# Optimization experiments

Hardware: AMD Instinct MI355X
Metric: run time of the kernel (lower is better)

## Reference

```python
import jax, jax.numpy as jnp
import numpy as np
import math

B, S, D, H, L, DFF = 64, 512, 512, 8, 2, 1024
DK = D // H
NEG = -1e32
LN_EPS = 1e-5


def cosine_pos_emb(seqlen, d_model):
    # pe[:,0::2]=sin(pos*div), pe[:,1::2]=cos(pos*div) -- fully overwrites the randn init
    pos = jnp.arange(seqlen, dtype=jnp.float32)[:, None]
    div = jnp.exp(jnp.arange(0, d_model, 2, dtype=jnp.float32) * (-math.log(10000.0) / d_model))
    ang = pos * div  # [S, D/2]
    return jnp.stack([jnp.sin(ang), jnp.cos(ang)], axis=-1).reshape(seqlen, d_model)


def layernorm(x, g, b):
    m = jnp.mean(x, axis=-1, keepdims=True)
    v = jnp.var(x, axis=-1, keepdims=True)
    return g * (x - m) * jax.lax.rsqrt(v + LN_EPS) + b


def setup_inputs() -> dict:
    key = jax.random.key(0)
    ks = jax.random.split(key, 8)
    sc = 0.02
    inp = {
        'q_embed_data': jax.random.normal(ks[0], (B, S, D), jnp.float32),
        'qa_embed_data': jax.random.normal(ks[1], (B, S, D), jnp.float32),
        'forget_rate': jax.random.uniform(ks[2], (B, 1, S, 1), jnp.float32),
        # per-block params, leading dim = n_blocks (kq_same=1: q uses k_linear)
        'Wk': jax.random.normal(ks[3], (L, D, D), jnp.float32) * sc,
        'bk': jnp.zeros((L, D), jnp.float32),
        'Wv': jax.random.normal(ks[4], (L, D, D), jnp.float32) * sc,
        'bv': jnp.zeros((L, D), jnp.float32),
        'Wo': jax.random.normal(ks[5], (L, D, D), jnp.float32) * sc,
        'bo': jnp.zeros((L, D), jnp.float32),
        'ln1_g': jnp.ones((L, D), jnp.float32),
        'ln1_b': jnp.zeros((L, D), jnp.float32),
        'W1': jax.random.normal(ks[6], (L, D, DFF), jnp.float32) * sc,
        'b1': jnp.zeros((L, DFF), jnp.float32),
        'W2': jax.random.normal(ks[7], (L, DFF, D), jnp.float32) * sc,
        'b2': jnp.zeros((L, D), jnp.float32),
        'ln2_g': jnp.ones((L, D), jnp.float32),
        'ln2_b': jnp.zeros((L, D), jnp.float32),
    }
    return inp


def reference(q_embed_data, qa_embed_data, forget_rate, Wk, bk, Wv, bv, Wo, bo,
              ln1_g, ln1_b, W1, b1, W2, b2, ln2_g, ln2_b):
    pe = cosine_pos_emb(S, D)
    x = q_embed_data + pe  # query/key stream
    y = qa_embed_data + pe  # value stream (fixed across blocks)
    # mask=0 path: np.triu(ones, k=0) == 0 -> strictly lower-triangular allowed
    allow = jnp.tril(jnp.ones((S, S), dtype=bool), -1)
    scale = 1.0 / math.sqrt(DK)
    for i in range(L):
        qk = (x @ Wk[i] + bk[i]).reshape(B, S, H, DK).transpose(0, 2, 1, 3)  # [B,H,S,dk]
        v = (y @ Wv[i] + bv[i]).reshape(B, S, H, DK).transpose(0, 2, 1, 3)
        scores = jnp.einsum('bhqd,bhkd->bhqk', qk, qk) * scale
        scores = scores * forget_rate  # [B,1,S,1] broadcasts over heads and keys
        scores = jnp.where(allow, scores, NEG)
        p = jax.nn.softmax(scores, axis=-1)
        p = p.at[:, :, 0, :].set(0.0)  # zero_pad: first query row zeroed
        attn = jnp.einsum('bhqk,bhkd->bhqd', p, v).transpose(0, 2, 1, 3).reshape(B, S, D)
        attn = attn @ Wo[i] + bo[i]
        x = layernorm(x + attn, ln1_g[i], ln1_b[i])
        ff = jax.nn.relu(x @ W1[i] + b1[i]) @ W2[i] + b2[i]
        x = layernorm(x + ff, ln2_g[i], ln2_b[i])
    return x
```

## Files before the change

### kernel.cpp

```cpp
#include <hip/hip_runtime.h>
#include <cstdio>

#define B_   64
#define S_   512
#define D_   512
#define H_   8
#define DK_  64
#define DFF_ 1024
#define L_   2
#define BS_  (B_ * S_)

typedef __attribute__((ext_vector_type(8))) short bf16x8;
typedef __attribute__((ext_vector_type(4))) short bf16x4;
typedef __attribute__((ext_vector_type(4))) float f32x4;

__device__ inline short f2bf(float f) {
  unsigned u = __float_as_uint(f);
  u = u + 0x7FFF + ((u >> 16) & 1);
  return (short)(u >> 16);
}
__device__ inline float bf2f(short s) {
  return __uint_as_float(((unsigned)(unsigned short)s) << 16);
}

__device__ inline void gl_lds16(const short* g, void* lds_base) {
  __builtin_amdgcn_global_load_lds(
      (const __attribute__((address_space(1))) void*)g,
      (__attribute__((address_space(3))) void*)lds_base, 16, 0, 0);
}

__global__ void pe_kernel(float* __restrict__ pe) {
  int idx = blockIdx.x * 256 + threadIdx.x;
  int s = idx >> 9, d = idx & 511;
  float dv = __expf((float)(d & ~1) * (-9.210340371976184f / (float)D_));
  float ang = (float)s * dv;
  pe[idx] = (d & 1) ? cosf(ang) : sinf(ang);
}

__global__ __launch_bounds__(256) void prep_kernel(
    const float* __restrict__ q, const float* __restrict__ qa,
    const float* __restrict__ pe,
    short* __restrict__ xb, short* __restrict__ yb) {
  size_t base = ((size_t)blockIdx.x * 256 + threadIdx.x) * 8;
  int sd = (int)(base & (size_t)(S_ * D_ - 1));
  f32x4 p0 = *(const f32x4*)(pe + sd);
  f32x4 p1 = *(const f32x4*)(pe + sd + 4);
  f32x4 q0 = *(const f32x4*)(q + base);
  f32x4 q1 = *(const f32x4*)(q + base + 4);
  f32x4 a0 = *(const f32x4*)(qa + base);
  f32x4 a1 = *(const f32x4*)(qa + base + 4);
  bf16x8 xv, yv;
#pragma unroll
  for (int i = 0; i < 4; ++i) {
    xv[i] = f2bf(q0[i] + p0[i]);
    yv[i] = f2bf(a0[i] + p0[i]);
  }
#pragma unroll
  for (int i = 0; i < 4; ++i) {
    xv[4 + i] = f2bf(q1[i] + p1[i]);
    yv[4 + i] = f2bf(a1[i] + p1[i]);
  }
  *(bf16x8*)(xb + base) = xv;
  *(bf16x8*)(yb + base) = yv;
}

struct TrArgs {
  const float* src[10];
  short* dst[10];
  int R[10], C[10];
};
__global__ __launch_bounds__(256) void tr_w_all(TrArgs a) {
  const int slot = blockIdx.z;
  const int R = a.R[slot], C = a.C[slot];
  const int c0 = blockIdx.x * 64, r0 = blockIdx.y * 64;
  if (c0 >= C || r0 >= R) return;
  const float* __restrict__ src = a.src[slot];
  short* __restrict__ dst = a.dst[slot];
  __shared__ short Ts[64][72];
  const int t = threadIdx.x;
#pragma unroll
  for (int it = 0; it < 2; ++it) {
    int c2 = it * 256 + t;
    int srow = c2 >> 3, schunk = c2 & 7;
    const float* sp = src + (size_t)(r0 + srow) * C + c0 + schunk * 8;
    f32x4 a0 = *(const f32x4*)sp;
    f32x4 a1 = *(const f32x4*)(sp + 4);
#pragma unroll
    for (int k = 0; k < 4; ++k) Ts[srow][schunk * 8 + k] = f2bf(a0[k]);
#pragma unroll
    for (int k = 0; k < 4; ++k) Ts[srow][schunk * 8 + 4 + k] = f2bf(a1[k]);
  }
  __syncthreads();
#pragma unroll
  for (int it = 0; it < 2; ++it) {
    int c2 = it * 256 + t;
    int orow = c2 >> 3, ochunk = c2 & 7;
    bf16x8 vv;
#pragma unroll
    for (int k = 0; k < 8; ++k) vv[k] = Ts[ochunk * 8 + k][orow];
    *(bf16x8*)(dst + (size_t)(c0 + orow) * R + r0 + ochunk * 8) = vv;
  }
}

__global__ __launch_bounds__(512, 2) void gemm_bt(
    const short* __restrict__ A, const short* __restrict__ BT,
    const float* __restrict__ bias, short* __restrict__ Cb,
    int M, int N, int K, int relu, int bias_row, int nx, int xmaj)
{
  const int nwg = gridDim.x;
  const int cpx = nwg >> 3;
  const int l = (blockIdx.x & 7) * cpx + (blockIdx.x >> 3);
  int bcol, brow;
  if (xmaj) { bcol = l % nx; brow = l / nx; }
  else      { int ny = nwg / nx; brow = l % ny; bcol = l / ny; }

  __shared__ __align__(16) short As[2][256 * 64];
  __shared__ __align__(16) short Bs[2][256 * 64];
  const int t = threadIdx.x;
  const int w = t >> 6, lane = t & 63, lr = lane & 15, lk = lane >> 4;
  const int wm = w >> 2, wn = w & 3;

  const f32x4 vzero = {0.f, 0.f, 0.f, 0.f};
  f32x4 acc[8][4];
#pragma unroll
  for (int m = 0; m < 8; ++m)
#pragma unroll
    for (int n = 0; n < 4; ++n) acc[m][n] = vzero;

  const short* Abase = A + (size_t)brow * 256 * K;
  const short* Bbase = BT + (size_t)bcol * 256 * K;

  auto stageH = [&](short* lds, const short* gsrc, int half, int k0) {
#pragma unroll
    for (int it = 0; it < 2; ++it) {
      int c = it * 512 + t;
      int cb = it * 512 + w * 64;
      int row = half * 128 + (c >> 3);
      int seg = (c & 7) ^ (row & 7);
      gl_lds16(gsrc + (size_t)row * K + k0 + seg * 8,
               (char*)lds + (size_t)(half * 1024 + cb) * 16);
    }
  };
  auto ldfrag = [&](const short* lds, int row, int s) -> bf16x8 {
    int chunk = row * 8 + (s ^ (row & 7));
    return *(const bf16x8*)((const char*)lds + (size_t)chunk * 16);
  };

  const int T = K >> 6;
  stageH(&As[0][0], Abase, 0, 0);
  stageH(&As[0][0], Abase, 1, 0);
  stageH(&Bs[0][0], Bbase, 0, 0);
  stageH(&Bs[0][0], Bbase, 1, 0);

  for (int ti = 0; ti < T; ++ti) {
    const int cbuf = ti & 1, obuf = cbuf ^ 1;
    asm volatile("s_waitcnt vmcnt(0)" ::: "memory");
    asm volatile("s_barrier" ::: "memory");

    if (ti + 1 < T) {
      int k1 = (ti + 1) * 64;
      stageH(&As[obuf][0], Abase, 0, k1);
      stageH(&As[obuf][0], Abase, 1, k1);
      stageH(&Bs[obuf][0], Bbase, 0, k1);
      stageH(&Bs[obuf][0], Bbase, 1, k1);
    }

    bf16x8 bf[4][2];
#pragma unroll
    for (int n = 0; n < 4; ++n)
#pragma unroll
      for (int kk = 0; kk < 2; ++kk)
        bf[n][kk] = ldfrag(&Bs[cbuf][0], wn * 64 + n * 16 + lr, kk * 4 + lk);

#pragma unroll
    for (int p = 0; p < 4; ++p) {
      bf16x8 af[2][2];
#pragma unroll
      for (int mm = 0; mm < 2; ++mm)
#pragma unroll
        for (int kk = 0; kk < 2; ++kk)
          af[mm][kk] = ldfrag(&As[cbuf][0], wm * 128 + (p * 2 + mm) * 16 + lr, kk * 4 + lk);
      __builtin_amdgcn_sched_barrier(0);
      __builtin_amdgcn_s_setprio(1);
#pragma unroll
      for (int mm = 0; mm < 2; ++mm)
#pragma unroll
        for (int n = 0; n < 4; ++n)
#pragma unroll
          for (int kk = 0; kk < 2; ++kk)
            acc[p * 2 + mm][n] = __builtin_amdgcn_mfma_f32_16x16x32_bf16(
                bf[n][kk], af[mm][kk], acc[p * 2 + mm][n], 0, 0, 0);
      __builtin_amdgcn_s_setprio(0);
      __builtin_amdgcn_sched_barrier(0);
      asm volatile("s_barrier" ::: "memory");
    }
  }

#pragma unroll
  for (int m = 0; m < 8; ++m) {
    int row = brow * 256 + wm * 128 + m * 16 + lr;
    float brv = (bias && bias_row) ? bias[row] : 0.f;
    size_t rb = (size_t)row * N;
#pragma unroll
    for (int n = 0; n < 4; ++n) {
      int colb = bcol * 256 + wn * 64 + n * 16 + lk * 4;
      f32x4 bv4;
      if (bias && !bias_row) bv4 = *(const f32x4*)(bias + colb);
      else { bv4[0] = brv; bv4[1] = brv; bv4[2] = brv; bv4[3] = brv; }
      bf16x4 ov;
#pragma unroll
      for (int j = 0; j < 4; ++j) {
        float vv = acc[m][n][j] + bv4[j];
        if (relu) vv = fmaxf(vv, 0.f);
        ov[j] = f2bf(vv);
      }
      *(bf16x4*)(Cb + rb + colb) = ov;
    }
  }
}

template<int P>
__device__ __forceinline__ void attn_body(
    const short* __restrict__ qk, const short* __restrict__ vT,
    const float* __restrict__ fr, short* __restrict__ out,
    short (*Pl)[552], float (*redsum)[32][4],
    int h, int b, int w, int lr, int lk)
{
  constexpr int qo0 = 32 * P, qo1 = 32 * (15 - P);
  constexpr int c0 = 2 * P + 2;
  constexpr int colb1 = c0 * 16;
  constexpr int n0 = P + 1;
  constexpr int n1 = 16 - P;

  const size_t qk_head = (size_t)b * S_ * D_ + (size_t)h * DK_;
  const float scale = 0.125f;

  bf16x8 qf0[2][2], qf1[2][2];
#pragma unroll
  for (int qt = 0; qt < 2; ++qt)
#pragma unroll
    for (int ks = 0; ks < 2; ++ks) {
      qf0[qt][ks] = *(const bf16x8*)(qk + qk_head + (size_t)(qo0 + qt * 16 + lr) * D_ + ks * 32 + lk * 8);
      qf1[qt][ks] = *(const bf16x8*)(qk + qk_head + (size_t)(qo1 + qt * 16 + lr) * D_ + ks * 32 + lk * 8);
    }

  float frv0[2], frv1[2];
#pragma unroll
  for (int qt = 0; qt < 2; ++qt) {
    frv0[qt] = scale * fr[(size_t)b * S_ + qo0 + qt * 16 + lr];
    frv1[qt] = scale * fr[(size_t)b * S_ + qo1 + qt * 16 + lr];
  }

  const f32x4 vzero = {0.f, 0.f, 0.f, 0.f};
  f32x4 acc[9][2];
#pragma unroll
  for (int i = 0; i < 9; ++i) { acc[i][0] = vzero; acc[i][1] = vzero; }

  const int nfr = (w < 2) ? 9 : 8;
  const short* kqbase = qk + qk_head + (size_t)lr * D_ + lk * 8;
  auto kfoff = [&](int i) -> size_t {
    int f = w + 4 * i;
    int kt = (f < c0) ? f : f - c0;
    return (size_t)kt * 16 * D_;
  };
  bf16x8 kreg[4][2];
#pragma unroll
  for (int i = 0; i < 4; ++i) {
    if (i < nfr) {
      const short* p = kqbase + kfoff(i);
      kreg[i][0] = *(const bf16x8*)p;
      kreg[i][1] = *(const bf16x8*)(p + 32);
    }
  }
  __builtin_amdgcn_sched_barrier(0);
#pragma unroll
  for (int i = 0; i < 9; ++i) {
    if (i < nfr) {
      const int f = w + 4 * i;
      __builtin_amdgcn_s_setprio(1);
      if (f < c0) {
#pragma unroll
        for (int ks = 0; ks < 2; ++ks) {
          acc[i][0] = __builtin_amdgcn_mfma_f32_16x16x32_bf16(kreg[i & 3][ks], qf0[0][ks], acc[i][0], 0, 0, 0);
          acc[i][1] = __builtin_amdgcn_mfma_f32_16x16x32_bf16(kreg[i & 3][ks], qf0[1][ks], acc[i][1], 0, 0, 0);
        }
      } else {
#pragma unroll
        for (int ks = 0; ks < 2; ++ks) {
          acc[i][0] = __builtin_amdgcn_mfma_f32_16x16x32_bf16(kreg[i & 3][ks], qf1[0][ks], acc[i][0], 0, 0, 0);
          acc[i][1] = __builtin_amdgcn_mfma_f32_16x16x32_bf16(kreg[i & 3][ks], qf1[1][ks], acc[i][1], 0, 0, 0);
        }
      }
      __builtin_amdgcn_s_setprio(0);
      __builtin_amdgcn_sched_barrier(0);
      if (i + 4 < nfr) {
        const short* p = kqbase + kfoff(i + 4);
        kreg[i & 3][0] = *(const bf16x8*)p;
        kreg[i & 3][1] = *(const bf16x8*)(p + 32);
      }
      __builtin_amdgcn_sched_barrier(0);
    }
  }

  const int uqt0 = w & 1, udh0 = w >> 1;
  const int uqt1 = w >> 1, udh1 = w & 1;
  const short* vu0 = vT + (size_t)(h * DK_ + udh0 * 32 + lr) * BS_ + (size_t)b * S_ + lk * 8;
  const short* vu1 = vT + (size_t)(h * DK_ + udh1 * 32 + lr) * BS_ + (size_t)b * S_ + lk * 8;
  bf16x8 vfB[3][2][2];
#pragma unroll
  for (int kb = 0; kb < 3; ++kb) {
    if (kb < n0) {
#pragma unroll
      for (int n = 0; n < 2; ++n)
        vfB[kb][0][n] = *(const bf16x8*)(vu0 + (size_t)n * 16 * BS_ + kb * 32);
    }
    if (kb < n1) {
#pragma unroll
      for (int n = 0; n < 2; ++n)
        vfB[kb][1][n] = *(const bf16x8*)(vu1 + (size_t)n * 16 * BS_ + kb * 32);
    }
  }
  __builtin_amdgcn_sched_barrier(0);

  float rs00 = 0.f, rs01 = 0.f, rs10 = 0.f, rs11 = 0.f;
#pragma unroll
  for (int frag = 0; frag < 34; ++frag) {
    if ((frag & 3) == w) {
      const int i = frag >> 2;
      const int tl = (frag < c0) ? 0 : 1;
      const int kt = tl ? frag - c0 : frag;
      const int kbase = kt * 16 + lk * 4;
      const int colb = (tl ? colb1 : 0) + kbase;
#pragma unroll
      for (int qt = 0; qt < 2; ++qt) {
        int qrow = (tl ? qo1 : qo0) + qt * 16 + lr;
        float fv = tl ? frv1[qt] : frv0[qt];
        bf16x4 pk;
        float rs = 0.f;
#pragma unroll
        for (int j = 0; j < 4; ++j) {
          float e = (kbase + j < qrow) ? __expf(acc[i][qt][j] * fv) : 0.f;
          rs += e;
          pk[j] = f2bf(e);
        }
        *(bf16x4*)&Pl[qt * 16 + lr][colb] = pk;
        if (tl == 0) { if (qt == 0) rs00 += rs; else rs01 += rs; }
        else         { if (qt == 0) rs10 += rs; else rs11 += rs; }
      }
    }
  }

#pragma unroll
  for (int msk = 16; msk < 64; msk <<= 1) {
    rs00 += __shfl_xor(rs00, msk);
    rs01 += __shfl_xor(rs01, msk);
    rs10 += __shfl_xor(rs10, msk);
    rs11 += __shfl_xor(rs11, msk);
  }
  if (lk == 0) {
    redsum[0][lr][w] = rs00;
    redsum[0][16 + lr][w] = rs01;
    redsum[1][lr][w] = rs10;
    redsum[1][16 + lr][w] = rs11;
  }
  __syncthreads();

  const short* prow0 = &Pl[uqt0 * 16 + lr][lk * 8];
  const short* prow1 = &Pl[uqt1 * 16 + lr][colb1 + lk * 8];
  f32x4 oacc0[2] = {vzero, vzero}, oacc1[2] = {vzero, vzero};
  bf16x8 paB[2][2];
  paB[0][0] = *(const bf16x8*)prow0;
  paB[0][1] = *(const bf16x8*)prow1;

#pragma unroll
  for (int kb = 0; kb < 16; ++kb) {
    const int sc = kb % 3, pc = kb & 1, pn = pc ^ 1;
    if (kb + 1 < n0) paB[pn][0] = *(const bf16x8*)(prow0 + (kb + 1) * 32);
    if (kb + 1 < n1) paB[pn][1] = *(const bf16x8*)(prow1 + (kb + 1) * 32);
    __builtin_amdgcn_sched_barrier(0);
    __builtin_amdgcn_s_setprio(1);
    if (kb < n0) {
#pragma unroll
      for (int n = 0; n < 2; ++n)
        oacc0[n] = __builtin_amdgcn_mfma_f32_16x16x32_bf16(paB[pc][0], vfB[sc][0][n], oacc0[n], 0, 0, 0);
    }
    if (kb < n1) {
#pragma unroll
      for (int n = 0; n < 2; ++n)
        oacc1[n] = __builtin_amdgcn_mfma_f32_16x16x32_bf16(paB[pc][1], vfB[sc][1][n], oacc1[n], 0, 0, 0);
    }
    __builtin_amdgcn_s_setprio(0);
    __builtin_amdgcn_sched_barrier(0);
    if (kb + 3 < n0) {
#pragma unroll
      for (int n = 0; n < 2; ++n)
        vfB[sc][0][n] = *(const bf16x8*)(vu0 + (size_t)n * 16 * BS_ + (kb + 3) * 32);
    }
    if (kb + 3 < n1) {
#pragma unroll
      for (int n = 0; n < 2; ++n)
        vfB[sc][1][n] = *(const bf16x8*)(vu1 + (size_t)n * 16 * BS_ + (kb + 3) * 32);
    }
    __builtin_amdgcn_sched_barrier(0);
  }

  {
    float invd[4];
#pragma unroll
    for (int j = 0; j < 4; ++j) {
      int row = uqt0 * 16 + lk * 4 + j;
      float ds = redsum[0][row][0] + redsum[0][row][1] + redsum[0][row][2] + redsum[0][row][3];
      invd[j] = ds > 0.f ? 1.f / ds : 0.f;
    }
#pragma unroll
    for (int n = 0; n < 2; ++n)
#pragma unroll
      for (int j = 0; j < 4; ++j) {
        int qrow = qo0 + uqt0 * 16 + lk * 4 + j;
        out[qk_head + (size_t)qrow * D_ + udh0 * 32 + n * 16 + lr] = f2bf(oacc0[n][j] * invd[j]);
      }
  }
  {
    float invd[4];
#pragma unroll
    for (int j = 0; j < 4; ++j) {
      int row = uqt1 * 16 + lk * 4 + j;
      float ds = redsum[1][row][0] + redsum[1][row][1] + redsum[1][row][2] + redsum[1][row][3];
      invd[j] = ds > 0.f ? 1.f / ds : 0.f;
    }
#pragma unroll
    for (int n = 0; n < 2; ++n)
#pragma unroll
      for (int j = 0; j < 4; ++j) {
        int qrow = qo1 + uqt1 * 16 + lk * 4 + j;
        out[qk_head + (size_t)qrow * D_ + udh1 * 32 + n * 16 + lr] = f2bf(oacc1[n][j] * invd[j]);
      }
  }
}

__global__ __launch_bounds__(256, 3) void attn_kernel(
    const short* __restrict__ qk, const short* __restrict__ vT,
    const float* __restrict__ fr, short* __restrict__ out)
{
  const int hw = blockIdx.x;
  const int l = (hw & 7) * 512 + (hw >> 3);
  const int p = l & 7, hb = l >> 3;
  const int h = hb & 7, b = hb >> 3;
  const int t = threadIdx.x;
  const int w = t >> 6, lr = t & 15, lk = (t & 63) >> 4;

  __shared__ __align__(16) short Pl[32][552];
  __shared__ __align__(16) float redsum[2][32][4];

  switch (p) {
    case 0: attn_body<0>(qk, vT, fr, out, Pl, redsum, h, b, w, lr, lk); break;
    case 1: attn_body<1>(qk, vT, fr, out, Pl, redsum, h, b, w, lr, lk); break;
    case 2: attn_body<2>(qk, vT, fr, out, Pl, redsum, h, b, w, lr, lk); break;
    case 3: attn_body<3>(qk, vT, fr, out, Pl, redsum, h, b, w, lr, lk); break;
    case 4: attn_body<4>(qk, vT, fr, out, Pl, redsum, h, b, w, lr, lk); break;
    case 5: attn_body<5>(qk, vT, fr, out, Pl, redsum, h, b, w, lr, lk); break;
    case 6: attn_body<6>(qk, vT, fr, out, Pl, redsum, h, b, w, lr, lk); break;
    case 7: attn_body<7>(qk, vT, fr, out, Pl, redsum, h, b, w, lr, lk); break;
  }
}

template<int FINAL>
__global__ __launch_bounds__(256) void ln_res_t(
    const short* __restrict__ xin, const short* __restrict__ add,
    const float* __restrict__ g, const float* __restrict__ bb,
    short* __restrict__ xbout, float* __restrict__ fout)
{
  const int row = blockIdx.x * 4 + (threadIdx.x >> 6);
  const int lane = threadIdx.x & 63;
  const size_t base = (size_t)row * D_ + lane * 8;

  bf16x8 xv = *(const bf16x8*)(xin + base);
  bf16x8 av = *(const bf16x8*)(add + base);
  float vals[8];
#pragma unroll
  for (int i = 0; i < 8; ++i) vals[i] = bf2f(xv[i]) + bf2f(av[i]);

  float s = 0.f, sq = 0.f;
#pragma unroll
  for (int i = 0; i < 8; ++i) { s += vals[i]; sq += vals[i] * vals[i]; }
#pragma unroll
  for (int m = 1; m < 64; m <<= 1) { s += __shfl_xor(s, m); sq += __shfl_xor(sq, m); }

  float mean = s * (1.f / D_);
  float var = sq * (1.f / D_) - mean * mean;
  float rstd = rsqrtf(var + 1e-5f);

  int col = lane * 8;
  if (FINAL) {
    f32x4 o0, o1;
#pragma unroll
    for (int i = 0; i < 8; ++i) {
      float vv = g[col + i] * (vals[i] - mean) * rstd + bb[col + i];
      if (i < 4) o0[i] = vv; else o1[i - 4] = vv;
    }
    *(f32x4*)(fout + base) = o0;
    *(f32x4*)(fout + base + 4) = o1;
  } else {
    bf16x8 ob;
#pragma unroll
    for (int i = 0; i < 8; ++i)
      ob[i] = f2bf(g[col + i] * (vals[i] - mean) * rstd + bb[col + i]);
    *(bf16x8*)(xbout + base) = ob;
  }
}

extern "C" void kernel_launch(void* const* d_in, const int* in_sizes, int n_in,
                              void* d_out, int out_size, void* d_ws, size_t ws_size,
                              hipStream_t stream) {
  const float* q_emb = (const float*)d_in[0];
  const float* qa_emb = (const float*)d_in[1];
  const float* frate = (const float*)d_in[2];
  const float* Wk = (const float*)d_in[3];
  const float* bk = (const float*)d_in[4];
  const float* Wv = (const float*)d_in[5];
  const float* bv = (const float*)d_in[6];
  const float* Wo = (const float*)d_in[7];
  const float* bo = (const float*)d_in[8];
  const float* ln1g = (const float*)d_in[9];
  const float* ln1b = (const float*)d_in[10];
  const float* W1 = (const float*)d_in[11];
  const float* b1 = (const float*)d_in[12];
  const float* W2 = (const float*)d_in[13];
  const float* b2 = (const float*)d_in[14];
  const float* ln2g = (const float*)d_in[15];
  const float* ln2b = (const float*)d_in[16];
  float* x = (float*)d_out;

  char* ws = (char*)d_ws;
  size_t off = 0;
  auto alloc = [&](size_t bytes) -> void* {
    void* p = ws + off;
    off += (bytes + 255) & ~(size_t)255;
    return p;
  };
  const size_t MTOK = (size_t)BS_;
  float* pe    = (float*)alloc((size_t)S_ * D_ * 4);
  short* xb    = (short*)alloc(MTOK * D_ * 2);
  short* yb    = (short*)alloc(MTOK * D_ * 2);
  short* qkb   = (short*)alloc(MTOK * D_ * 2);
  short* vTb   = (short*)alloc(MTOK * D_ * 2);
  short* ff1b  = (short*)alloc(MTOK * DFF_ * 2);
  short* attnb = ff1b;
  short* goutb = qkb;
  short* wT[L_][5];
  for (int i = 0; i < L_; ++i) {
    wT[i][0] = (short*)alloc((size_t)D_ * D_ * 2);
    wT[i][1] = (short*)alloc((size_t)D_ * D_ * 2);
    wT[i][2] = (short*)alloc((size_t)D_ * D_ * 2);
    wT[i][3] = (short*)alloc((size_t)D_ * DFF_ * 2);
    wT[i][4] = (short*)alloc((size_t)DFF_ * D_ * 2);
  }
  if (off > ws_size) {
    fprintf(stderr, "parKT: workspace overflow: need %zu have %zu\n", off, ws_size);
    return;
  }

  pe_kernel<<<(S_ * D_) / 256, 256, 0, stream>>>(pe);
  prep_kernel<<<(int)(MTOK * D_ / (256 * 8)), 256, 0, stream>>>(q_emb, qa_emb, pe, xb, yb);

  TrArgs ta;
  for (int i = 0; i < L_; ++i) {
    ta.src[i * 5 + 0] = Wk + (size_t)i * D_ * D_;  ta.dst[i * 5 + 0] = wT[i][0]; ta.R[i * 5 + 0] = D_;   ta.C[i * 5 + 0] = D_;
    ta.src[i * 5 + 1] = Wv + (size_t)i * D_ * D_;  ta.dst[i * 5 + 1] = wT[i][1]; ta.R[i * 5 + 1] = D_;   ta.C[i * 5 + 1] = D_;
    ta.src[i * 5 + 2] = Wo + (size_t)i * D_ * D_;  ta.dst[i * 5 + 2] = wT[i][2]; ta.R[i * 5 + 2] = D_;   ta.C[i * 5 + 2] = D_;
    ta.src[i * 5 + 3] = W1 + (size_t)i * D_ * DFF_; ta.dst[i * 5 + 3] = wT[i][3]; ta.R[i * 5 + 3] = D_;   ta.C[i * 5 + 3] = DFF_;
    ta.src[i * 5 + 4] = W2 + (size_t)i * DFF_ * D_; ta.dst[i * 5 + 4] = wT[i][4]; ta.R[i * 5 + 4] = DFF_; ta.C[i * 5 + 4] = D_;
  }
  tr_w_all<<<dim3(DFF_ / 64, DFF_ / 64, 10), 256, 0, stream>>>(ta);

  const int M = (int)MTOK;
  for (int i = 0; i < L_; ++i) {
    gemm_bt<<<(M / 256) * (D_ / 256), 512, 0, stream>>>(xb, wT[i][0], bk + (size_t)i * D_, qkb, M, D_, D_, 0, 0, D_ / 256, 1);
    gemm_bt<<<(D_ / 256) * (M / 256), 512, 0, stream>>>(wT[i][1], yb, bv + (size_t)i * D_, vTb, D_, M, D_, 0, 1, M / 256, 0);
    attn_kernel<<<(S_ / 64) * H_ * B_, 256, 0, stream>>>(qkb, vTb, frate, attnb);
    gemm_bt<<<(M / 256) * (D_ / 256), 512, 0, stream>>>(attnb, wT[i][2], bo + (size_t)i * D_, goutb, M, D_, D_, 0, 0, D_ / 256, 1);
    ln_res_t<0><<<M / 4, 256, 0, stream>>>(xb, goutb, ln1g + (size_t)i * D_, ln1b + (size_t)i * D_, xb, nullptr);
    gemm_bt<<<(M / 256) * (DFF_ / 256), 512, 0, stream>>>(xb, wT[i][3], b1 + (size_t)i * DFF_, ff1b, M, DFF_, D_, 1, 0, DFF_ / 256, 1);
    gemm_bt<<<(M / 256) * (D_ / 256), 512, 0, stream>>>(ff1b, wT[i][4], b2 + (size_t)i * D_, goutb, M, D_, DFF_, 0, 0, D_ / 256, 1);
    if (i == L_ - 1)
      ln_res_t<1><<<M / 4, 256, 0, stream>>>(xb, goutb, ln2g + (size_t)i * D_, ln2b + (size_t)i * D_, nullptr, x);
    else
      ln_res_t<0><<<M / 4, 256, 0, stream>>>(xb, goutb, ln2g + (size_t)i * D_, ln2b + (size_t)i * D_, xb, nullptr);
  }
}
```

Measured before the change: 735.0 us.

## Merge QK and V projections into one GEMM launch and pipeline K-halves

The QK and transposed-V projection GEMMs now run as a single grouped launch: each workgroup picks its problem from a pair of argument structs by block index. The GEMM main loop is restructured so LDS is laid out per 32-wide K half with a new swizzle. The next tile's loads are issued in quarter-steps interleaved with the MFMA blocks, with partial vmcnt waits instead of a full drain. This aims to overlap global-to-LDS traffic with compute and to cut one launch plus its tail per layer. The cost is more complex waitcnt accounting, which risks reading data before it has arrived if the counts are wrong.

```diff
diff --git a/kernel.cpp b/kernel.cpp
--- a/kernel.cpp
+++ b/kernel.cpp
@@ -102,20 +102,33 @@
   }
 }
 
-__global__ __launch_bounds__(512, 2) void gemm_bt(
-    const short* __restrict__ A, const short* __restrict__ BT,
-    const float* __restrict__ bias, short* __restrict__ Cb,
-    int M, int N, int K, int relu, int bias_row, int nx, int xmaj)
+struct GArgs {
+  const short* A; const short* BT; const float* bias; short* Cb;
+  int M, N, K, relu, bias_row, nx, xmaj, nblk;
+};
+__global__ __launch_bounds__(512, 2) void gemm_bt2(GArgs g0, GArgs g1)
 {
   const int nwg = gridDim.x;
   const int cpx = nwg >> 3;
   const int l = (blockIdx.x & 7) * cpx + (blockIdx.x >> 3);
+
+  const short* A; const short* BT; const float* bias; short* Cb;
+  int N, K, relu, bias_row, nx, xmaj, ll, nb;
+  if (l < g0.nblk) {
+    A = g0.A; BT = g0.BT; bias = g0.bias; Cb = g0.Cb;
+    N = g0.N; K = g0.K; relu = g0.relu; bias_row = g0.bias_row;
+    nx = g0.nx; xmaj = g0.xmaj; ll = l; nb = g0.nblk;
+  } else {
+    A = g1.A; BT = g1.BT; bias = g1.bias; Cb = g1.Cb;
+    N = g1.N; K = g1.K; relu = g1.relu; bias_row = g1.bias_row;
+    nx = g1.nx; xmaj = g1.xmaj; ll = l - g0.nblk; nb = g1.nblk;
+  }
   int bcol, brow;
-  if (xmaj) { bcol = l % nx; brow = l / nx; }
-  else      { int ny = nwg / nx; brow = l % ny; bcol = l / ny; }
-
-  __shared__ __align__(16) short As[2][256 * 64];
-  __shared__ __align__(16) short Bs[2][256 * 64];
+  if (xmaj) { bcol = ll % nx; brow = ll / nx; }
+  else      { int ny = nb / nx; brow = ll % ny; bcol = ll / ny; }
+
+  __shared__ __align__(16) short As[2][16384];
+  __shared__ __align__(16) short Bs[2][16384];
   const int t = threadIdx.x;
   const int w = t >> 6, lane = t & 63, lr = lane & 15, lk = lane >> 4;
   const int wm = w >> 2, wn = w & 3;
@@ -130,70 +143,96 @@
   const short* Abase = A + (size_t)brow * 256 * K;
   const short* Bbase = BT + (size_t)bcol * 256 * K;
 
-  auto stageH = [&](short* lds, const short* gsrc, int half, int k0) {
+  auto stageH = [&](short* ldsbuf, const short* gsrc, int kk, int k0) {
 #pragma unroll
     for (int it = 0; it < 2; ++it) {
       int c = it * 512 + t;
       int cb = it * 512 + w * 64;
-      int row = half * 128 + (c >> 3);
-      int seg = (c & 7) ^ (row & 7);
-      gl_lds16(gsrc + (size_t)row * K + k0 + seg * 8,
-               (char*)lds + (size_t)(half * 1024 + cb) * 16);
+      int row = c >> 2, pos = c & 3;
+      int gc = pos ^ ((row >> 1) & 3);
+      gl_lds16(gsrc + (size_t)row * K + k0 + kk * 32 + gc * 8,
+               (char*)ldsbuf + (size_t)(kk * 1024 + cb) * 16);
     }
   };
-  auto ldfrag = [&](const short* lds, int row, int s) -> bf16x8 {
-    int chunk = row * 8 + (s ^ (row & 7));
-    return *(const bf16x8*)((const char*)lds + (size_t)chunk * 16);
+  auto ldfrag = [&](const short* ldsbuf, int kk, int row) -> bf16x8 {
+    int chunk = kk * 1024 + row * 4 + (lk ^ ((row >> 1) & 3));
+    return *(const bf16x8*)((const char*)ldsbuf + (size_t)chunk * 16);
   };
 
   const int T = K >> 6;
-  stageH(&As[0][0], Abase, 0, 0);
-  stageH(&As[0][0], Abase, 1, 0);
-  stageH(&Bs[0][0], Bbase, 0, 0);
-  stageH(&Bs[0][0], Bbase, 1, 0);
+  stageH(As[0], Abase, 0, 0);
+  stageH(Bs[0], Bbase, 0, 0);
+  stageH(As[0], Abase, 1, 0);
+  stageH(Bs[0], Bbase, 1, 0);
 
   for (int ti = 0; ti < T; ++ti) {
     const int cbuf = ti & 1, obuf = cbuf ^ 1;
-    asm volatile("s_waitcnt vmcnt(0)" ::: "memory");
+    const int k1 = (ti + 1) * 64;
+    const bool more = (ti + 1 < T);
+
+    asm volatile("s_waitcnt vmcnt(4)" ::: "memory");
     asm volatile("s_barrier" ::: "memory");
 
-    if (ti + 1 < T) {
-      int k1 = (ti + 1) * 64;
-      stageH(&As[obuf][0], Abase, 0, k1);
-      stageH(&As[obuf][0], Abase, 1, k1);
-      stageH(&Bs[obuf][0], Bbase, 0, k1);
-      stageH(&Bs[obuf][0], Bbase, 1, k1);
-    }
-
-    bf16x8 bf[4][2];
-#pragma unroll
-    for (int n = 0; n < 4; ++n)
-#pragma unroll
-      for (int kk = 0; kk < 2; ++kk)
-        bf[n][kk] = ldfrag(&Bs[cbuf][0], wn * 64 + n * 16 + lr, kk * 4 + lk);
-
-#pragma unroll
-    for (int p = 0; p < 4; ++p) {
-      bf16x8 af[2][2];
-#pragma unroll
-      for (int mm = 0; mm < 2; ++mm)
-#pragma unroll
-        for (int kk = 0; kk < 2; ++kk)
-          af[mm][kk] = ldfrag(&As[cbuf][0], wm * 128 + (p * 2 + mm) * 16 + lr, kk * 4 + lk);
-      __builtin_amdgcn_sched_barrier(0);
-      __builtin_amdgcn_s_setprio(1);
-#pragma unroll
-      for (int mm = 0; mm < 2; ++mm)
-#pragma unroll
-        for (int n = 0; n < 4; ++n)
-#pragma unroll
-          for (int kk = 0; kk < 2; ++kk)
-            acc[p * 2 + mm][n] = __builtin_amdgcn_mfma_f32_16x16x32_bf16(
-                bf[n][kk], af[mm][kk], acc[p * 2 + mm][n], 0, 0, 0);
-      __builtin_amdgcn_s_setprio(0);
-      __builtin_amdgcn_sched_barrier(0);
-      asm volatile("s_barrier" ::: "memory");
-    }
+    if (more) stageH(As[obuf], Abase, 0, k1);
+    bf16x8 bf[4], af[4];
+#pragma unroll
+    for (int n = 0; n < 4; ++n) bf[n] = ldfrag(Bs[cbuf], 0, wn * 64 + n * 16 + lr);
+#pragma unroll
+    for (int m = 0; m < 4; ++m) af[m] = ldfrag(As[cbuf], 0, wm * 128 + m * 16 + lr);
+    __builtin_amdgcn_sched_barrier(0);
+    __builtin_amdgcn_s_setprio(1);
+#pragma unroll
+    for (int m = 0; m < 4; ++m)
+#pragma unroll
+      for (int n = 0; n < 4; ++n)
+        acc[m][n] = __builtin_amdgcn_mfma_f32_16x16x32_bf16(bf[n], af[m], acc[m][n], 0, 0, 0);
+    __builtin_amdgcn_s_setprio(0);
+    __builtin_amdgcn_sched_barrier(0);
+
+    if (more) stageH(Bs[obuf], Bbase, 0, k1);
+#pragma unroll
+    for (int m = 0; m < 4; ++m) af[m] = ldfrag(As[cbuf], 0, wm * 128 + (m + 4) * 16 + lr);
+    __builtin_amdgcn_sched_barrier(0);
+    __builtin_amdgcn_s_setprio(1);
+#pragma unroll
+    for (int m = 0; m < 4; ++m)
+#pragma unroll
+      for (int n = 0; n < 4; ++n)
+        acc[m + 4][n] = __builtin_amdgcn_mfma_f32_16x16x32_bf16(bf[n], af[m], acc[m + 4][n], 0, 0, 0);
+    __builtin_amdgcn_s_setprio(0);
+    __builtin_amdgcn_sched_barrier(0);
+
+    if (more) asm volatile("s_waitcnt vmcnt(4)" ::: "memory");
+    else      asm volatile("s_waitcnt vmcnt(0)" ::: "memory");
+    asm volatile("s_barrier" ::: "memory");
+
+    if (more) stageH(As[obuf], Abase, 1, k1);
+#pragma unroll
+    for (int n = 0; n < 4; ++n) bf[n] = ldfrag(Bs[cbuf], 1, wn * 64 + n * 16 + lr);
+#pragma unroll
+    for (int m = 0; m < 4; ++m) af[m] = ldfrag(As[cbuf], 1, wm * 128 + m * 16 + lr);
+    __builtin_amdgcn_sched_barrier(0);
+    __builtin_amdgcn_s_setprio(1);
+#pragma unroll
+    for (int m = 0; m < 4; ++m)
+#pragma unroll
+      for (int n = 0; n < 4; ++n)
+        acc[m][n] = __builtin_amdgcn_mfma_f32_16x16x32_bf16(bf[n], af[m], acc[m][n], 0, 0, 0);
+    __builtin_amdgcn_s_setprio(0);
+    __builtin_amdgcn_sched_barrier(0);
+
+    if (more) stageH(Bs[obuf], Bbase, 1, k1);
+#pragma unroll
+    for (int m = 0; m < 4; ++m) af[m] = ldfrag(As[cbuf], 1, wm * 128 + (m + 4) * 16 + lr);
+    __builtin_amdgcn_sched_barrier(0);
+    __builtin_amdgcn_s_setprio(1);
+#pragma unroll
+    for (int m = 0; m < 4; ++m)
+#pragma unroll
+      for (int n = 0; n < 4; ++n)
+        acc[m + 4][n] = __builtin_amdgcn_mfma_f32_16x16x32_bf16(bf[n], af[m], acc[m + 4][n], 0, 0, 0);
+    __builtin_amdgcn_s_setprio(0);
+    __builtin_amdgcn_sched_barrier(0);
   }
 
 #pragma unroll
@@ -574,14 +613,30 @@
   tr_w_all<<<dim3(DFF_ / 64, DFF_ / 64, 10), 256, 0, stream>>>(ta);
 
   const int M = (int)MTOK;
+  const GArgs gempty = {nullptr, nullptr, nullptr, nullptr, 0, 0, 0, 0, 0, 1, 1, 0};
   for (int i = 0; i < L_; ++i) {
-    gemm_bt<<<(M / 256) * (D_ / 256), 512, 0, stream>>>(xb, wT[i][0], bk + (size_t)i * D_, qkb, M, D_, D_, 0, 0, D_ / 256, 1);
-    gemm_bt<<<(D_ / 256) * (M / 256), 512, 0, stream>>>(wT[i][1], yb, bv + (size_t)i * D_, vTb, D_, M, D_, 0, 1, M / 256, 0);
+    GArgs gqk = {xb, wT[i][0], bk + (size_t)i * D_, qkb,
+                 M, D_, D_, 0, 0, D_ / 256, 1, (M / 256) * (D_ / 256)};
+    GArgs gvt = {wT[i][1], yb, bv + (size_t)i * D_, vTb,
+                 D_, M, D_, 0, 1, (D_ / 256) * (M / 256) / (D_ / 256), 0, (D_ / 256) * (M / 256)};
+    gvt.nx = gvt.nblk / (D_ / 256);
+    gemm_bt2<<<gqk.nblk + gvt.nblk, 512, 0, stream>>>(gqk, gvt);
+
     attn_kernel<<<(S_ / 64) * H_ * B_, 256, 0, stream>>>(qkb, vTb, frate, attnb);
-    gemm_bt<<<(M / 256) * (D_ / 256), 512, 0, stream>>>(attnb, wT[i][2], bo + (size_t)i * D_, goutb, M, D_, D_, 0, 0, D_ / 256, 1);
+
+    GArgs gwo = {attnb, wT[i][2], bo + (size_t)i * D_, goutb,
+                 M, D_, D_, 0, 0, D_ / 256, 1, (M / 256) * (D_ / 256)};
+    gemm_bt2<<<gwo.nblk, 512, 0, stream>>>(gwo, gempty);
     ln_res_t<0><<<M / 4, 256, 0, stream>>>(xb, goutb, ln1g + (size_t)i * D_, ln1b + (size_t)i * D_, xb, nullptr);
-    gemm_bt<<<(M / 256) * (DFF_ / 256), 512, 0, stream>>>(xb, wT[i][3], b1 + (size_t)i * DFF_, ff1b, M, DFF_, D_, 1, 0, DFF_ / 256, 1);
-    gemm_bt<<<(M / 256) * (D_ / 256), 512, 0, stream>>>(ff1b, wT[i][4], b2 + (size_t)i * D_, goutb, M, D_, DFF_, 0, 0, D_ / 256, 1);
+
+    GArgs gf1 = {xb, wT[i][3], b1 + (size_t)i * DFF_, ff1b,
+                 M, DFF_, D_, 1, 0, DFF_ / 256, 1, (M / 256) * (DFF_ / 256)};
+    gemm_bt2<<<gf1.nblk, 512, 0, stream>>>(gf1, gempty);
+
+    GArgs gf2 = {ff1b, wT[i][4], b2 + (size_t)i * D_, goutb,
+                 M, D_, DFF_, 0, 0, D_ / 256, 1, (M / 256) * (D_ / 256)};
+    gemm_bt2<<<gf2.nblk, 512, 0, stream>>>(gf2, gempty);
+
     if (i == L_ - 1)
       ln_res_t<1><<<M / 4, 256, 0, stream>>>(xb, goutb, ln2g + (size_t)i * D_, ln2b + (size_t)i * D_, nullptr, x);
     else
```

After: 725.3 us. About the same (-1.3%).
